# Kernel tuning notes

Hardware: AMD Instinct MI355X
Metric: run time of the kernel (lower is better)

Reference implementation:

```python
import jax, jax.numpy as jnp
import numpy as np

OUT_H = 512
OUT_W = 512
GRID_SIZE = 3
N = GRID_SIZE * GRID_SIZE  # number of TPS control points
BATCH = 32


def setup_inputs() -> dict:
    key = jax.random.key(0)
    # theta = [Q_X (N), Q_Y (N), P_X (N), P_Y (N)]
    theta = jax.random.normal(key, (BATCH, 4 * N), dtype=jnp.float32)
    return {"theta": theta}


def _compute_L_inverse(PX, PY):
    # PX, PY: [B, N] control point coordinates
    d2 = (PX[:, :, None] - PX[:, None, :]) ** 2 + (PY[:, :, None] - PY[:, None, :]) ** 2
    d2 = jnp.where(d2 == 0, 1.0, d2)
    K = d2 * jnp.log(d2)                                        # [B, N, N]
    O = jnp.ones((PX.shape[0], N, 1), dtype=PX.dtype)
    P = jnp.concatenate([O, PX[:, :, None], PY[:, :, None]], axis=2)  # [B, N, 3]
    Z = jnp.zeros((PX.shape[0], 3, 3), dtype=PX.dtype)
    L = jnp.concatenate([
        jnp.concatenate([K, P], axis=2),
        jnp.concatenate([jnp.swapaxes(P, 1, 2), Z], axis=2),
    ], axis=1)                                                  # [B, N+3, N+3]
    return jnp.linalg.inv(L)


def reference(theta):
    # theta: [B, 4N]
    QX = theta[:, :N]
    QY = theta[:, N:2 * N]
    PX = theta[:, 2 * N:3 * N]
    PY = theta[:, 3 * N:]

    Li = _compute_L_inverse(PX, PY)                             # [B, N+3, N+3]
    WX = jnp.einsum('bij,bj->bi', Li[:, :N, :N], QX)            # [B, N]
    WY = jnp.einsum('bij,bj->bi', Li[:, :N, :N], QY)
    AX = jnp.einsum('bij,bj->bi', Li[:, N:, :N], QX)            # [B, 3]
    AY = jnp.einsum('bij,bj->bi', Li[:, N:, :N], QY)

    gx = jnp.linspace(-1.0, 1.0, OUT_W, dtype=theta.dtype)
    gy = jnp.linspace(-1.0, 1.0, OUT_H, dtype=theta.dtype)
    GX, GY = jnp.meshgrid(gx, gy)                               # [H, W]

    # squared distances from every pixel to every control point: [B, H, W, N]
    d2 = (GX[None, :, :, None] - PX[:, None, None, :]) ** 2 \
       + (GY[None, :, :, None] - PY[:, None, None, :]) ** 2
    d2 = jnp.where(d2 == 0, 1.0, d2)
    U = d2 * jnp.log(d2)

    xp = (AX[:, 0, None, None]
          + AX[:, 1, None, None] * GX[None]
          + AX[:, 2, None, None] * GY[None]
          + jnp.einsum('bhwn,bn->bhw', U, WX))                  # [B, H, W]
    yp = (AY[:, 0, None, None]
          + AY[:, 1, None, None] * GX[None]
          + AY[:, 2, None, None] * GY[None]
          + jnp.einsum('bhwn,bn->bhw', U, WY))

    return jnp.stack([xp, yp], axis=-1)                         # [B, H, W, 2]
```

## Files before the change

### kernel.cpp

```cpp
#include <hip/hip_runtime.h>
#include <math.h>

#define NCTRL 9
#define DIM 12
#define NCOLS (DIM + 2)
#define OUT_H 512
#define OUT_W 512
#define BATCH 32

typedef float nfloat4 __attribute__((ext_vector_type(4)));

__global__ __launch_bounds__(64) void tps_solve_kernel(
    const float* __restrict__ theta, float* __restrict__ coef) {
    const int b = blockIdx.x;
    const int lane = threadIdx.x;
    const float* th = theta + b * 36;

    __shared__ double M[DIM][NCOLS + 1];
    __shared__ double fshare[DIM];

    for (int e = lane; e < DIM * NCOLS; e += 64) {
        const int r = e / NCOLS;
        const int c = e % NCOLS;
        double v;
        if (c < DIM) {
            if (r < NCTRL && c < NCTRL) {
                const double dx = (double)th[18 + r] - (double)th[18 + c];
                const double dy = (double)th[27 + r] - (double)th[27 + c];
                const double d2 = dx * dx + dy * dy;
                v = (d2 == 0.0) ? 0.0 : d2 * log(d2);
            } else if (r < NCTRL) {
                v = (c == 9) ? 1.0 : (c == 10 ? (double)th[18 + r] : (double)th[27 + r]);
            } else if (c < NCTRL) {
                v = (r == 9) ? 1.0 : (r == 10 ? (double)th[18 + c] : (double)th[27 + c]);
            } else {
                v = 0.0;
            }
        } else if (c == DIM) {
            v = (r < NCTRL) ? (double)th[r] : 0.0;
        } else {
            v = (r < NCTRL) ? (double)th[9 + r] : 0.0;
        }
        M[r][c] = v;
    }
    __syncthreads();

    for (int k = 0; k < DIM; ++k) {
        double mv = (lane >= k && lane < DIM) ? fabs(M[lane][k]) : -1.0;
        int mi = lane;
        #pragma unroll
        for (int off = 8; off > 0; off >>= 1) {
            const double ov = __shfl_xor(mv, off);
            const int oi = __shfl_xor(mi, off);
            if (ov > mv) { mv = ov; mi = oi; }
        }
        mi = __shfl(mi, 0);
        if (mi != k && lane < NCOLS) {
            const double tmp = M[k][lane];
            M[k][lane] = M[mi][lane];
            M[mi][lane] = tmp;
        }
        __syncthreads();

        const double piv = M[k][k];
        if (lane < DIM && lane != k) fshare[lane] = M[lane][k] / piv;
        __syncthreads();

        for (int e = lane; e < DIM * NCOLS; e += 64) {
            const int r = e / NCOLS;
            const int c = e % NCOLS;
            if (r != k && c >= k) M[r][c] -= fshare[r] * M[k][c];
        }
        __syncthreads();
    }

    if (lane < DIM) {
        const double x = M[lane][DIM] / M[lane][lane];
        const double y = M[lane][DIM + 1] / M[lane][lane];
        float* cb = coef + b * 24;
        if (lane < NCTRL) {
            cb[lane] = (float)x;
            cb[9 + lane] = (float)y;
        } else {
            cb[18 + (lane - 9)] = (float)x;
            cb[21 + (lane - 9)] = (float)y;
        }
    }
}

__global__ __launch_bounds__(256) void tps_grid_kernel(
    const float* __restrict__ theta, const float* __restrict__ coef,
    float* __restrict__ out) {
    const int b = blockIdx.y;
    const float* th = theta + b * 36;
    const float* cf = coef + b * 24;

    float PX[NCTRL], PY[NCTRL], WX[NCTRL], WY[NCTRL];
    #pragma unroll
    for (int n = 0; n < NCTRL; ++n) {
        PX[n] = th[18 + n];
        PY[n] = th[27 + n];
        WX[n] = cf[n];
        WY[n] = cf[9 + n];
    }
    const float AX0 = cf[18], AX1 = cf[19], AX2 = cf[20];
    const float AY0 = cf[21], AY1 = cf[22], AY2 = cf[23];

    const int t = threadIdx.x;
    const int row0 = blockIdx.x * 4;
    const int col0 = t * 2;

    const float step = 2.0f / 511.0f;
    const float gx0 = -1.0f + step * (float)col0;
    const float gx1 = gx0 + step;
    const float gy0 = -1.0f + step * (float)row0;

    float xp[8], yp[8];
    #pragma unroll
    for (int q = 0; q < 4; ++q) {
        const float gy = gy0 + step * (float)q;
        xp[q * 2 + 0] = AX0 + AX1 * gx0 + AX2 * gy;
        yp[q * 2 + 0] = AY0 + AY1 * gx0 + AY2 * gy;
        xp[q * 2 + 1] = AX0 + AX1 * gx1 + AX2 * gy;
        yp[q * 2 + 1] = AY0 + AY1 * gx1 + AY2 * gy;
    }

    #pragma unroll
    for (int n = 0; n < NCTRL; ++n) {
        const float dx0 = gx0 - PX[n];
        const float dx1 = dx0 + step;
        const float dx0sq = dx0 * dx0;
        const float dx1sq = dx1 * dx1;
        float dy = gy0 - PY[n];
        #pragma unroll
        for (int q = 0; q < 4; ++q) {
            const float r20 = __builtin_fmaf(dy, dy, dx0sq);
            const float r21 = __builtin_fmaf(dy, dy, dx1sq);
            const float u0 = r20 * __logf(fmaxf(r20, 1e-30f));
            const float u1 = r21 * __logf(fmaxf(r21, 1e-30f));
            xp[q * 2 + 0] = __builtin_fmaf(u0, WX[n], xp[q * 2 + 0]);
            yp[q * 2 + 0] = __builtin_fmaf(u0, WY[n], yp[q * 2 + 0]);
            xp[q * 2 + 1] = __builtin_fmaf(u1, WX[n], xp[q * 2 + 1]);
            yp[q * 2 + 1] = __builtin_fmaf(u1, WY[n], yp[q * 2 + 1]);
            dy += step;
        }
    }

    #pragma unroll
    for (int q = 0; q < 4; ++q) {
        const size_t off =
            (((size_t)b * OUT_H + (size_t)(row0 + q)) * OUT_W + (size_t)col0) * 2;
        nfloat4 o = {xp[q * 2], yp[q * 2], xp[q * 2 + 1], yp[q * 2 + 1]};
        __builtin_nontemporal_store(o, (nfloat4*)(out + off));
    }
}

extern "C" void kernel_launch(void* const* d_in, const int* in_sizes, int n_in,
                              void* d_out, int out_size, void* d_ws, size_t ws_size,
                              hipStream_t stream) {
    const float* theta = (const float*)d_in[0];
    float* out = (float*)d_out;
    float* coef = (float*)d_ws;

    tps_solve_kernel<<<dim3(BATCH), dim3(64), 0, stream>>>(theta, coef);

    tps_grid_kernel<<<dim3(OUT_H / 4, BATCH), dim3(256), 0, stream>>>(theta, coef, out);
}
```

Before: 109.5 us.

## Solve TPS systems in registers with shuffles, four batches per wavefront

```diff
diff --git a/kernel.cpp b/kernel.cpp
--- a/kernel.cpp
+++ b/kernel.cpp
@@ -3,7 +3,6 @@
 
 #define NCTRL 9
 #define DIM 12
-#define NCOLS (DIM + 2)
 #define OUT_H 512
 #define OUT_W 512
 #define BATCH 32
@@ -12,78 +11,80 @@
 
 __global__ __launch_bounds__(64) void tps_solve_kernel(
     const float* __restrict__ theta, float* __restrict__ coef) {
-    const int b = blockIdx.x;
     const int lane = threadIdx.x;
+    const int g = lane >> 4;
+    const int r = lane & 15;
+    const int b = blockIdx.x * 4 + g;
     const float* th = theta + b * 36;
 
-    __shared__ double M[DIM][NCOLS + 1];
-    __shared__ double fshare[DIM];
+    const bool arow = (r < DIM);
 
-    for (int e = lane; e < DIM * NCOLS; e += 64) {
-        const int r = e / NCOLS;
-        const int c = e % NCOLS;
-        double v;
-        if (c < DIM) {
-            if (r < NCTRL && c < NCTRL) {
-                const double dx = (double)th[18 + r] - (double)th[18 + c];
-                const double dy = (double)th[27 + r] - (double)th[27 + c];
-                const double d2 = dx * dx + dy * dy;
-                v = (d2 == 0.0) ? 0.0 : d2 * log(d2);
-            } else if (r < NCTRL) {
-                v = (c == 9) ? 1.0 : (c == 10 ? (double)th[18 + r] : (double)th[27 + r]);
-            } else if (c < NCTRL) {
-                v = (r == 9) ? 1.0 : (r == 10 ? (double)th[18 + c] : (double)th[27 + c]);
-            } else {
-                v = 0.0;
-            }
-        } else if (c == DIM) {
-            v = (r < NCTRL) ? (double)th[r] : 0.0;
-        } else {
-            v = (r < NCTRL) ? (double)th[9 + r] : 0.0;
-        }
-        M[r][c] = v;
+    double M[14];
+    double pxr = 0.0, pyr = 0.0;
+    if (r < NCTRL) { pxr = (double)th[18 + r]; pyr = (double)th[27 + r]; }
+
+    #pragma unroll
+    for (int c = 0; c < NCTRL; ++c) {
+        const double pxc = (double)th[18 + c];
+        const double pyc = (double)th[27 + c];
+        double v = 0.0;
+        if (r < NCTRL) {
+            const double dx = pxr - pxc;
+            const double dy = pyr - pyc;
+            const double d2 = dx * dx + dy * dy;
+            v = (d2 == 0.0) ? 0.0 : d2 * log(d2);
+        } else if (r == 9)  v = 1.0;
+        else if (r == 10)   v = pxc;
+        else if (r == 11)   v = pyc;
+        M[c] = v;
     }
-    __syncthreads();
+    if (r < NCTRL) {
+        M[9] = 1.0; M[10] = pxr; M[11] = pyr;
+        M[12] = (double)th[r];
+        M[13] = (double)th[NCTRL + r];
+    } else {
+        M[9] = 0.0; M[10] = 0.0; M[11] = 0.0;
+        M[12] = 0.0; M[13] = 0.0;
+    }
 
+    bool done = false;
+    int mycol = -1;
+    double pivdiag = 1.0;
+
+    #pragma unroll
     for (int k = 0; k < DIM; ++k) {
-        double mv = (lane >= k && lane < DIM) ? fabs(M[lane][k]) : -1.0;
-        int mi = lane;
+        double mv = (arow && !done) ? fabs(M[k]) : -1.0;
+        int mi = r;
         #pragma unroll
         for (int off = 8; off > 0; off >>= 1) {
             const double ov = __shfl_xor(mv, off);
             const int oi = __shfl_xor(mi, off);
-            if (ov > mv) { mv = ov; mi = oi; }
+            if (ov > mv || (ov == mv && oi < mi)) { mv = ov; mi = oi; }
         }
-        mi = __shfl(mi, 0);
-        if (mi != k && lane < NCOLS) {
-            const double tmp = M[k][lane];
-            M[k][lane] = M[mi][lane];
-            M[mi][lane] = tmp;
+        const int src = (g << 4) | mi;
+        const double pkk = __shfl(M[k], src);
+        const double rp = 1.0 / pkk;
+        const double f = M[k] * rp;
+        const bool ispiv = (r == mi);
+        if (ispiv) { done = true; mycol = k; pivdiag = pkk; }
+        #pragma unroll
+        for (int c = k + 1; c < 14; ++c) {
+            const double Pc = __shfl(M[c], src);
+            if (!ispiv) M[c] -= f * Pc;
         }
-        __syncthreads();
-
-        const double piv = M[k][k];
-        if (lane < DIM && lane != k) fshare[lane] = M[lane][k] / piv;
-        __syncthreads();
-
-        for (int e = lane; e < DIM * NCOLS; e += 64) {
-            const int r = e / NCOLS;
-            const int c = e % NCOLS;
-            if (r != k && c >= k) M[r][c] -= fshare[r] * M[k][c];
-        }
-        __syncthreads();
     }
 
-    if (lane < DIM) {
-        const double x = M[lane][DIM] / M[lane][lane];
-        const double y = M[lane][DIM + 1] / M[lane][lane];
+    if (mycol >= 0) {
+        const double inv = 1.0 / pivdiag;
+        const float x = (float)(M[12] * inv);
+        const float y = (float)(M[13] * inv);
         float* cb = coef + b * 24;
-        if (lane < NCTRL) {
-            cb[lane] = (float)x;
-            cb[9 + lane] = (float)y;
+        if (mycol < NCTRL) {
+            cb[mycol] = x;
+            cb[9 + mycol] = y;
         } else {
-            cb[18 + (lane - 9)] = (float)x;
-            cb[21 + (lane - 9)] = (float)y;
+            cb[18 + (mycol - 9)] = x;
+            cb[21 + (mycol - 9)] = y;
         }
     }
 }
@@ -162,7 +163,7 @@
     float* out = (float*)d_out;
     float* coef = (float*)d_ws;
 
-    tps_solve_kernel<<<dim3(BATCH), dim3(64), 0, stream>>>(theta, coef);
+    tps_solve_kernel<<<dim3(BATCH / 4), dim3(64), 0, stream>>>(theta, coef);
 
     tps_grid_kernel<<<dim3(OUT_H / 4, BATCH), dim3(256), 0, stream>>>(theta, coef, out);
 }
```

Result: no change. 108.0 us (-1.4%).
